# Performance work log

Hardware: AMD Instinct MI355X
Metric: run time of the kernel (lower is better)

## Reference

```python
import jax, jax.numpy as jnp
import numpy as np

N = 30000
SLOPE = 0.2  # PyG GATConv default negative_slope


def _gat_conv(x, src, dst, W, a_src, a_dst, b, heads, out_ch, concat):
    """PyG GATConv (add_self_loops already applied), eval mode (no dropout).
    x: [N, F_in]; src/dst: [E] int; W: [F_in, heads*out_ch];
    a_src/a_dst: [heads, out_ch]; b: [heads*out_ch] or [out_ch]."""
    n = x.shape[0]
    h = (x @ W).reshape(n, heads, out_ch)              # [N, H, C]
    al_src = jnp.sum(h * a_src, axis=-1)               # [N, H]
    al_dst = jnp.sum(h * a_dst, axis=-1)               # [N, H]
    e = jax.nn.leaky_relu(al_src[src] + al_dst[dst], SLOPE)  # [E, H]
    # segment softmax over incoming edges of each destination node
    m = jax.ops.segment_max(e, dst, num_segments=n)
    ex = jnp.exp(e - m[dst])
    denom = jax.ops.segment_sum(ex, dst, num_segments=n)
    alpha = ex / (denom[dst] + 1e-16)                  # [E, H]
    msg = h[src] * alpha[..., None]                    # [E, H, C]
    out = jax.ops.segment_sum(msg, dst, num_segments=n)  # [N, H, C]
    out = out.reshape(n, heads * out_ch) if concat else out.mean(axis=1)
    return out + b


def setup_inputs() -> dict:
    key = jax.random.key(0)
    ks = jax.random.split(key, 20)
    E = 480000
    IN, H0, H1, LAT = 256, 64, 128, 32
    HEADS = 4
    x = jax.random.normal(ks[0], (N, IN), dtype=jnp.float32)
    edge_index = jax.random.randint(ks[1], (2, E), 0, N, dtype=jnp.int32)

    def gp(k, fin, heads, outc, concat):
        k1, k2, k3, k4 = jax.random.split(k, 4)
        s = 0.1
        W = jax.random.normal(k1, (fin, heads * outc), dtype=jnp.float32) * s
        a_s = jax.random.normal(k2, (heads, outc), dtype=jnp.float32) * s
        a_d = jax.random.normal(k3, (heads, outc), dtype=jnp.float32) * s
        b = jax.random.normal(k4, (heads * outc if concat else outc,), dtype=jnp.float32) * s
        return W, a_s, a_d, b

    W1, as1, ad1, b1 = gp(ks[2], IN, HEADS, H0, True)
    W2, as2, ad2, b2 = gp(ks[3], H0 * HEADS, HEADS, H1, True)
    Wm, asm, adm, bm = gp(ks[4], H1 * HEADS, HEADS, LAT, False)
    Wl, asl, adl, bl = gp(ks[5], H1 * HEADS, HEADS, LAT, False)
    return dict(x=x, edge_index=edge_index,
                W1=W1, as1=as1, ad1=ad1, b1=b1,
                W2=W2, as2=as2, ad2=ad2, b2=b2,
                Wm=Wm, asm=asm, adm=adm, bm=bm,
                Wl=Wl, asl=asl, adl=adl, bl=bl)


def reference(x, edge_index, W1, as1, ad1, b1, W2, as2, ad2, b2,
              Wm, asm, adm, bm, Wl, asl, adl, bl):
    n = x.shape[0]
    # add self loops (PyG GATConv default)
    loop = jnp.arange(n, dtype=edge_index.dtype)
    src = jnp.concatenate([edge_index[0], loop])
    dst = jnp.concatenate([edge_index[1], loop])

    out = _gat_conv(x, src, dst, W1, as1, ad1, b1, heads=4, out_ch=64, concat=True)
    out = jax.nn.relu(out)
    out = _gat_conv(out, src, dst, W2, as2, ad2, b2, heads=4, out_ch=128, concat=True)
    out = jax.nn.relu(out)
    # F.dropout with training=False (eval) is identity
    z_mean = _gat_conv(out, src, dst, Wm, asm, adm, bm, heads=4, out_ch=32, concat=False)
    z_logstd = _gat_conv(out, src, dst, Wl, asl, adl, bl, heads=4, out_ch=32, concat=False)
    return z_mean, z_logstd
```

## Files before the change

### kernel.cpp

```cpp
#include <hip/hip_runtime.h>
#include <cstddef>

typedef __attribute__((ext_vector_type(8))) short short8;
typedef __attribute__((ext_vector_type(4))) float f32x4;
typedef __attribute__((ext_vector_type(8))) _Float16 half8;
typedef __attribute__((ext_vector_type(2))) _Float16 half2v;

union H8 { half8 v; half2v p[4]; unsigned int w[4]; };
union W1H2 { unsigned int w; half2v p; };

__device__ __forceinline__ unsigned short f2h(float f) {
    union { _Float16 h; unsigned short u; } x; x.h = (_Float16)f; return x.u;
}
__device__ __forceinline__ float h2f(unsigned short u) {
    union { unsigned short u; _Float16 h; } x; x.u = u; return (float)x.h;
}
__device__ __forceinline__ float lrelu(float v) { return v > 0.f ? v : 0.2f * v; }


__global__ void count_edges_kernel(const int* __restrict__ ei, int E, int N,
                                   int* __restrict__ cnt) {
    int e = blockIdx.x * blockDim.x + threadIdx.x;
    if (e >= E + N) return;
    int d = (e < E) ? ei[E + e] : (e - E);
    atomicAdd(&cnt[d], 1);
}


__global__ void scan_p1_kernel(const int* __restrict__ cnt, int* __restrict__ rp,
                               int* __restrict__ bsum, int n) {
    __shared__ int sh[256];
    int t = threadIdx.x, i = blockIdx.x * 256 + t;
    sh[t] = (i < n) ? cnt[i] : 0;
    __syncthreads();
    for (int off = 1; off < 256; off <<= 1) {
        int u = (t >= off) ? sh[t - off] : 0;
        __syncthreads();
        sh[t] += u;
        __syncthreads();
    }
    if (i < n) rp[i + 1] = sh[t];
    if (t == 255) bsum[blockIdx.x] = sh[255];
}

__global__ void scan_p2_kernel(int* __restrict__ bsum, int nb) {
    __shared__ int sh[256];
    int t = threadIdx.x;
    sh[t] = (t < nb) ? bsum[t] : 0;
    __syncthreads();
    for (int off = 1; off < 256; off <<= 1) {
        int u = (t >= off) ? sh[t - off] : 0;
        __syncthreads();
        sh[t] += u;
        __syncthreads();
    }
    if (t < nb) bsum[t] = (t == 0) ? 0 : sh[t - 1];
}

__global__ void scan_p3_kernel(int* __restrict__ rp, const int* __restrict__ bsum,
                               int* __restrict__ cnt, int n) {
    int i = blockIdx.x * 256 + threadIdx.x;
    if (i < n) {
        rp[i + 1] += bsum[blockIdx.x];
        cnt[i] = 0;
    }
    if (i == 0) rp[0] = 0;
}

__global__ void scatter_edges_kernel(const int* __restrict__ ei, int E, int N,
                                     const int* __restrict__ rp, int* __restrict__ cur,
                                     int* __restrict__ csrc) {
    int e = blockIdx.x * blockDim.x + threadIdx.x;
    if (e >= E + N) return;
    int s, d;
    if (e < E) { s = ei[e]; d = ei[E + e]; } else { s = e - E; d = s; }
    int pos = rp[d] + atomicAdd(&cur[d], 1);
    csrc[pos] = s;
}


__global__ void f32_to_f16_pad4_kernel(const float* __restrict__ in,
                                       unsigned short* __restrict__ out,
                                       int rows, int cols, int padRows) {
    int i = blockIdx.x * blockDim.x + threadIdx.x;
    int total = (padRows * cols) >> 2;
    if (i >= total) return;
    int r = (i * 4) / cols;
    ushort4 o;
    if (r < rows) {
        float4 v = *(const float4*)(in + (size_t)i * 4);
        o = make_ushort4(f2h(v.x), f2h(v.y), f2h(v.z), f2h(v.w));
    } else {
        o = make_ushort4(0, 0, 0, 0);
    }
    *(ushort4*)(out + (size_t)i * 4) = o;
}

__global__ void transpose_all_kernel(
    const float* __restrict__ W1, const float* __restrict__ W2,
    const float* __restrict__ Wm, const float* __restrict__ Wl,
    unsigned short* __restrict__ W1t, unsigned short* __restrict__ W2t,
    unsigned short* __restrict__ WmlT) {
    int i = blockIdx.x * blockDim.x + threadIdx.x;
    if (i < 65536) {
        int k = i >> 8, n = i & 255;
        W1t[(size_t)n * 256 + k] = f2h(W1[i]);
    } else if (i < 65536 + 131072) {
        int j = i - 65536;
        int k = j >> 9, n = j & 511;
        W2t[(size_t)n * 256 + k] = f2h(W2[j]);
    } else if (i < 65536 + 131072 + 65536) {
        int j = i - 196608;
        int k = j >> 7, n = j & 127;
        WmlT[(size_t)n * 512 + k] = f2h(Wm[j]);
    } else if (i < 65536 + 131072 + 131072) {
        int j = i - 262144;
        int k = j >> 7, n = j & 127;
        WmlT[(size_t)(128 + n) * 512 + k] = f2h(Wl[j]);
    }
}


__global__ __launch_bounds__(256) void gemm_f16_kernel(
    const unsigned short* __restrict__ A, const unsigned short* __restrict__ Bt,
    unsigned short* __restrict__ C, int M, int K, int Nc,
    float* __restrict__ al_s, float* __restrict__ al_d,
    const float* __restrict__ aslo, const float* __restrict__ adlo,
    const float* __restrict__ ashi, const float* __restrict__ adhi,
    int csplit, int Chead, int H) {
    __shared__ short As[64 * 32];
    __shared__ short Bs[128 * 32];
    __shared__ float salS[64][4];
    __shared__ float salD[64][4];
    int tid = threadIdx.x;
    int bm = blockIdx.y * 64;
    int bn = blockIdx.x * 128;
    int wave = tid >> 6, lane = tid & 63;
    int wm = (wave >> 1) * 32, wn = (wave & 1) * 64;
    int lm = lane & 15, lq = lane >> 4;

    f32x4 acc[2][4] = {};

    int c0 = tid, c1 = tid + 256;
    const unsigned short* Ap0 = A + (size_t)(bm + (c0 >> 2)) * K + (c0 & 3) * 8;
    const unsigned short* Bp0 = Bt + (size_t)(bn + (c0 >> 2)) * K + (c0 & 3) * 8;
    const unsigned short* Bp1 = Bt + (size_t)(bn + (c1 >> 2)) * K + (c1 & 3) * 8;

    short8 a0 = *(const short8*)(Ap0);
    short8 b0 = *(const short8*)(Bp0);
    short8 b1 = *(const short8*)(Bp1);

    for (int kk = 0; kk < K; kk += 32) {
        __syncthreads();
        *(short8*)&As[c0 * 8] = a0;
        *(short8*)&Bs[c0 * 8] = b0;
        *(short8*)&Bs[c1 * 8] = b1;
        if (kk + 32 < K) {
            a0 = *(const short8*)(Ap0 + kk + 32);
            b0 = *(const short8*)(Bp0 + kk + 32);
            b1 = *(const short8*)(Bp1 + kk + 32);
        }
        __syncthreads();
        half8 af[2], bf[4];
#pragma unroll
        for (int t = 0; t < 2; t++)
            af[t] = *(const half8*)&As[(wm + t * 16 + lm) * 32 + lq * 8];
#pragma unroll
        for (int t = 0; t < 4; t++)
            bf[t] = *(const half8*)&Bs[(wn + t * 16 + lm) * 32 + lq * 8];
#pragma unroll
        for (int tm = 0; tm < 2; tm++)
#pragma unroll
            for (int tn = 0; tn < 4; tn++)
                acc[tm][tn] = __builtin_amdgcn_mfma_f32_16x16x32_f16(
                    af[tm], bf[tn], acc[tm][tn], 0, 0, 0);
    }

#pragma unroll
    for (int tm = 0; tm < 2; tm++) {
#pragma unroll
        for (int r = 0; r < 4; r++) {
            int row = bm + wm + tm * 16 + lq * 4 + r;
            if (row < M) {
#pragma unroll
                for (int tn = 0; tn < 4; tn++) {
                    int col = bn + wn + tn * 16 + lm;
                    C[(size_t)row * Nc + col] = f2h(acc[tm][tn][r]);
                }
            }
        }
    }

    float asv[4], adv[4];
#pragma unroll
    for (int tn = 0; tn < 4; tn++) {
        int col = bn + wn + tn * 16 + lm;
        bool hi = col >= csplit;
        int cc = hi ? col - csplit : col;
        asv[tn] = hi ? ashi[cc] : aslo[cc];
        adv[tn] = hi ? adhi[cc] : adlo[cc];
    }
    int gb = wn >> 5;
#pragma unroll
    for (int tm = 0; tm < 2; tm++) {
#pragma unroll
        for (int r = 0; r < 4; r++) {
#pragma unroll
            for (int p = 0; p < 2; p++) {
                float s1 = acc[tm][2 * p][r] * asv[2 * p]
                         + acc[tm][2 * p + 1][r] * asv[2 * p + 1];
                float s2 = acc[tm][2 * p][r] * adv[2 * p]
                         + acc[tm][2 * p + 1][r] * adv[2 * p + 1];
#pragma unroll
                for (int off = 8; off >= 1; off >>= 1) {
                    s1 += __shfl_xor(s1, off);
                    s2 += __shfl_xor(s2, off);
                }
                if (lm == 0) {
                    int rl = wm + tm * 16 + lq * 4 + r;
                    salS[rl][gb + p] = s1;
                    salD[rl][gb + p] = s2;
                }
            }
        }
    }
    __syncthreads();
    if (tid < 64) {
        int row = bm + tid;
        if (row < M) {
            int hb = bn / Chead;
            int HB = 128 / Chead;
            int GH = Chead >> 5;
            for (int i = 0; i < HB; i++) {
                float ss = 0.f, sd = 0.f;
                for (int j = 0; j < GH; j++) {
                    ss += salS[tid][i * GH + j];
                    sd += salD[tid][i * GH + j];
                }
                al_s[(size_t)row * H + hb + i] = ss;
                al_d[(size_t)row * H + hb + i] = sd;
            }
        }
    }
}


template <int H4>
__global__ __launch_bounds__(256) void alpha_kernel(
    const int* __restrict__ rp, const int* __restrict__ csrc,
    const float* __restrict__ al_s, const float* __restrict__ al_d,
    unsigned short* __restrict__ alphaT, int Ep, int N) {
    const int H = 4 * H4;
    int wv = threadIdx.x >> 6;
    int lane = threadIdx.x & 63;
    int n = blockIdx.x * 4 + wv;
    if (n >= N) return;
    int beg = rp[n], end = rp[n + 1];
    int deg = end - beg;

    float ad[H];
#pragma unroll
    for (int g = 0; g < H4; g++)
        *(float4*)&ad[g * 4] = *(const float4*)(al_d + (size_t)n * H + g * 4);

    if (deg <= 64) {
        bool act = lane < deg;
        int s = act ? csrc[beg + lane] : 0;
        float v[H], m[H], ex[H], sum[H];
#pragma unroll
        for (int g = 0; g < H4; g++) {
            float4 as = *(const float4*)(al_s + (size_t)s * H + g * 4);
            v[g * 4 + 0] = lrelu(as.x + ad[g * 4 + 0]);
            v[g * 4 + 1] = lrelu(as.y + ad[g * 4 + 1]);
            v[g * 4 + 2] = lrelu(as.z + ad[g * 4 + 2]);
            v[g * 4 + 3] = lrelu(as.w + ad[g * 4 + 3]);
        }
#pragma unroll
        for (int j = 0; j < H; j++) m[j] = act ? v[j] : -3.402823466e38f;
#pragma unroll
        for (int off = 32; off >= 1; off >>= 1)
#pragma unroll
            for (int j = 0; j < H; j++) m[j] = fmaxf(m[j], __shfl_xor(m[j], off));
#pragma unroll
        for (int j = 0; j < H; j++) {
            ex[j] = act ? __expf(v[j] - m[j]) : 0.f;
            sum[j] = ex[j];
        }
#pragma unroll
        for (int off = 32; off >= 1; off >>= 1)
#pragma unroll
            for (int j = 0; j < H; j++) sum[j] += __shfl_xor(sum[j], off);
        if (act) {
#pragma unroll
            for (int j = 0; j < H; j++)
                alphaT[(size_t)j * Ep + beg + lane] = f2h(ex[j] / (sum[j] + 1e-16f));
        }
    } else {
        float m[H], sum[H];
#pragma unroll
        for (int j = 0; j < H; j++) m[j] = -3.402823466e38f;
        for (int e = beg + lane; e < end; e += 64) {
            int s = csrc[e];
#pragma unroll
            for (int g = 0; g < H4; g++) {
                float4 as = *(const float4*)(al_s + (size_t)s * H + g * 4);
                m[g * 4 + 0] = fmaxf(m[g * 4 + 0], lrelu(as.x + ad[g * 4 + 0]));
                m[g * 4 + 1] = fmaxf(m[g * 4 + 1], lrelu(as.y + ad[g * 4 + 1]));
                m[g * 4 + 2] = fmaxf(m[g * 4 + 2], lrelu(as.z + ad[g * 4 + 2]));
                m[g * 4 + 3] = fmaxf(m[g * 4 + 3], lrelu(as.w + ad[g * 4 + 3]));
            }
        }
#pragma unroll
        for (int off = 32; off >= 1; off >>= 1)
#pragma unroll
            for (int j = 0; j < H; j++) m[j] = fmaxf(m[j], __shfl_xor(m[j], off));
#pragma unroll
        for (int j = 0; j < H; j++) sum[j] = 0.f;
        for (int e = beg + lane; e < end; e += 64) {
            int s = csrc[e];
#pragma unroll
            for (int g = 0; g < H4; g++) {
                float4 as = *(const float4*)(al_s + (size_t)s * H + g * 4);
                sum[g * 4 + 0] += __expf(lrelu(as.x + ad[g * 4 + 0]) - m[g * 4 + 0]);
                sum[g * 4 + 1] += __expf(lrelu(as.y + ad[g * 4 + 1]) - m[g * 4 + 1]);
                sum[g * 4 + 2] += __expf(lrelu(as.z + ad[g * 4 + 2]) - m[g * 4 + 2]);
                sum[g * 4 + 3] += __expf(lrelu(as.w + ad[g * 4 + 3]) - m[g * 4 + 3]);
            }
        }
#pragma unroll
        for (int off = 32; off >= 1; off >>= 1)
#pragma unroll
            for (int j = 0; j < H; j++) sum[j] += __shfl_xor(sum[j], off);
        float r[H];
#pragma unroll
        for (int j = 0; j < H; j++) r[j] = 1.0f / (sum[j] + 1e-16f);
        for (int e = beg + lane; e < end; e += 64) {
            int s = csrc[e];
#pragma unroll
            for (int g = 0; g < H4; g++) {
                float4 as = *(const float4*)(al_s + (size_t)s * H + g * 4);
                alphaT[(size_t)(g * 4 + 0) * Ep + e] =
                    f2h(__expf(lrelu(as.x + ad[g * 4 + 0]) - m[g * 4 + 0]) * r[g * 4 + 0]);
                alphaT[(size_t)(g * 4 + 1) * Ep + e] =
                    f2h(__expf(lrelu(as.y + ad[g * 4 + 1]) - m[g * 4 + 1]) * r[g * 4 + 1]);
                alphaT[(size_t)(g * 4 + 2) * Ep + e] =
                    f2h(__expf(lrelu(as.z + ad[g * 4 + 2]) - m[g * 4 + 2]) * r[g * 4 + 2]);
                alphaT[(size_t)(g * 4 + 3) * Ep + e] =
                    f2h(__expf(lrelu(as.w + ad[g * 4 + 3]) - m[g * 4 + 3]) * r[g * 4 + 3]);
            }
        }
    }
}


template <int NS, int HC, int C>
__global__ __launch_bounds__(256) void agg_stage_kernel(
    const int* __restrict__ rp, const int* __restrict__ csrc,
    const unsigned short* __restrict__ alphaT, int Ep,
    const unsigned short* __restrict__ h, const float* __restrict__ bias,
    unsigned short* __restrict__ out, int N) {
    constexpr int NG = 32;
    constexpr int MAXE = 1024;
    __shared__ int lds_rp[NG + 1];
    __shared__ uint2 lds_ea[MAXE];
    int tid = threadIdx.x;
    int bs = blockIdx.x % NS;
    int g0 = (blockIdx.x / NS) * NG;
    const int hd = (bs * 64) / C;
    if (tid <= NG) {
        int nn = g0 + tid;
        lds_rp[tid] = rp[nn <= N ? nn : N];
    }
    __syncthreads();
    int e0 = lds_rp[0], span = lds_rp[NG] - e0;
    const unsigned short* at = alphaT + (size_t)hd * Ep + e0;
    bool fits = span <= MAXE;
    if (fits) {
        for (int i = tid; i < span; i += 256) {
            unsigned int off = (unsigned int)csrc[e0 + i] * (unsigned int)(HC * 2);
            unsigned int a = at[i];
            lds_ea[i] = make_uint2(off, a | (a << 16));
        }
    }
    __syncthreads();

    int grp = tid >> 3;
    int lg = tid & 7;
    int n = g0 + grp;
    if (n >= N) return;
    int ch = bs * 64 + lg * 8;
    const unsigned int lo = (unsigned int)ch * 2;
    const char* hb = (const char*)h;
    H8 A; A.v = half8{};

    if (fits) {
        int t = lds_rp[grp] - e0, end = lds_rp[grp + 1] - e0;
        for (; t + 3 < end; t += 4) {
            uint2 ea0 = lds_ea[t],     ea1 = lds_ea[t + 1];
            uint2 ea2 = lds_ea[t + 2], ea3 = lds_ea[t + 3];
            H8 h0, h1, h2, h3;
            h0.v = *(const half8*)(hb + (ea0.x + lo));
            h1.v = *(const half8*)(hb + (ea1.x + lo));
            h2.v = *(const half8*)(hb + (ea2.x + lo));
            h3.v = *(const half8*)(hb + (ea3.x + lo));
            W1H2 a0, a1, a2, a3;
            a0.w = ea0.y; a1.w = ea1.y; a2.w = ea2.y; a3.w = ea3.y;
#pragma unroll
            for (int i = 0; i < 4; i++) A.p[i] += h0.p[i] * a0.p;
#pragma unroll
            for (int i = 0; i < 4; i++) A.p[i] += h1.p[i] * a1.p;
#pragma unroll
            for (int i = 0; i < 4; i++) A.p[i] += h2.p[i] * a2.p;
#pragma unroll
            for (int i = 0; i < 4; i++) A.p[i] += h3.p[i] * a3.p;
        }
        for (; t < end; t++) {
            uint2 ea0 = lds_ea[t];
            W1H2 a0; a0.w = ea0.y;
            H8 h0; h0.v = *(const half8*)(hb + (ea0.x + lo));
#pragma unroll
            for (int i = 0; i < 4; i++) A.p[i] += h0.p[i] * a0.p;
        }
    } else {
        const unsigned short* atg = alphaT + (size_t)hd * Ep;
        for (int t = lds_rp[grp]; t < lds_rp[grp + 1]; t++) {
            unsigned int off = (unsigned int)csrc[t] * (unsigned int)(HC * 2);
            unsigned int a = atg[t];
            W1H2 a0; a0.w = a | (a << 16);
            H8 h0; h0.v = *(const half8*)(hb + (off + lo));
#pragma unroll
            for (int i = 0; i < 4; i++) A.p[i] += h0.p[i] * a0.p;
        }
    }

    short8 o;
#pragma unroll
    for (int i = 0; i < 8; i++)
        o[i] = (short)f2h(fmaxf((float)A.v[i] + bias[ch + i], 0.f));
    *(short8*)(out + (size_t)n * HC + ch) = o;
}


__global__ __launch_bounds__(256) void agg_mean_stage_kernel(
    const int* __restrict__ rp, const int* __restrict__ csrc,
    const unsigned short* __restrict__ alphaT, int Ep,
    const unsigned short* __restrict__ h,
    const float* __restrict__ bias1, const float* __restrict__ bias2,
    float* __restrict__ out1, float* __restrict__ out2, int N) {
    constexpr int NG = 16;
    constexpr int MAXE = 1024;
    __shared__ int lds_rp[NG + 1];
    __shared__ unsigned int lds_off[MAXE];
    __shared__ unsigned int lds_aw[4][MAXE];
    int tid = threadIdx.x;
    int o = blockIdx.x & 1;
    int g0 = (blockIdx.x >> 1) * NG;
    if (tid <= NG) {
        int nn = g0 + tid;
        lds_rp[tid] = rp[nn <= N ? nn : N];
    }
    __syncthreads();
    int e0 = lds_rp[0], span = lds_rp[NG] - e0;
    bool fits = span <= MAXE;
    if (fits) {
        for (int i = tid; i < span; i += 256)
            lds_off[i] = (unsigned int)csrc[e0 + i] * 512u;
#pragma unroll
        for (int hh = 0; hh < 4; hh++) {
            const unsigned short* at = alphaT + (size_t)(o * 4 + hh) * Ep + e0;
            for (int i = tid; i < span; i += 256) {
                unsigned int a = at[i];
                lds_aw[hh][i] = a | (a << 16);
            }
        }
    }
    __syncthreads();

    int grp = tid >> 4;
    int cg = tid & 15;
    int hh = cg >> 2;
    int n = g0 + grp;
    if (n >= N) return;
    int ch = o * 128 + cg * 8;
    const unsigned int lo = (unsigned int)ch * 2;
    const char* hb = (const char*)h;
    H8 A; A.v = half8{};

    if (fits) {
        int t = lds_rp[grp] - e0, end = lds_rp[grp + 1] - e0;
        for (; t + 3 < end; t += 4) {
            unsigned int o0 = lds_off[t],     o1 = lds_off[t + 1];
            unsigned int o2 = lds_off[t + 2], o3 = lds_off[t + 3];
            H8 h0, h1, h2, h3;
            h0.v = *(const half8*)(hb + (o0 + lo));
            h1.v = *(const half8*)(hb + (o1 + lo));
            h2.v = *(const half8*)(hb + (o2 + lo));
            h3.v = *(const half8*)(hb + (o3 + lo));
            W1H2 a0, a1, a2, a3;
            a0.w = lds_aw[hh][t];     a1.w = lds_aw[hh][t + 1];
            a2.w = lds_aw[hh][t + 2]; a3.w = lds_aw[hh][t + 3];
#pragma unroll
            for (int i = 0; i < 4; i++) A.p[i] += h0.p[i] * a0.p;
#pragma unroll
            for (int i = 0; i < 4; i++) A.p[i] += h1.p[i] * a1.p;
#pragma unroll
            for (int i = 0; i < 4; i++) A.p[i] += h2.p[i] * a2.p;
#pragma unroll
            for (int i = 0; i < 4; i++) A.p[i] += h3.p[i] * a3.p;
        }
        for (; t < end; t++) {
            W1H2 a0; a0.w = lds_aw[hh][t];
            H8 h0; h0.v = *(const half8*)(hb + (lds_off[t] + lo));
#pragma unroll
            for (int i = 0; i < 4; i++) A.p[i] += h0.p[i] * a0.p;
        }
    } else {
        const unsigned short* atg = alphaT + (size_t)(o * 4 + hh) * Ep;
        for (int t = lds_rp[grp]; t < lds_rp[grp + 1]; t++) {
            unsigned int off = (unsigned int)csrc[t] * 512u;
            unsigned int a = atg[t];
            W1H2 a0; a0.w = a | (a << 16);
            H8 h0; h0.v = *(const half8*)(hb + (off + lo));
#pragma unroll
            for (int i = 0; i < 4; i++) A.p[i] += h0.p[i] * a0.p;
        }
    }

    float f[8];
#pragma unroll
    for (int i = 0; i < 8; i++) f[i] = (float)A.v[i];
#pragma unroll
    for (int off = 4; off <= 8; off <<= 1)
#pragma unroll
        for (int i = 0; i < 8; i++) f[i] += __shfl_xor(f[i], off);
    if (cg < 4) {
        const float* bb = o ? bias2 : bias1;
        float* op = o ? out2 : out1;
        int wc = cg * 8;
        float4 r0, r1;
        r0.x = f[0] * 0.25f + bb[wc + 0];
        r0.y = f[1] * 0.25f + bb[wc + 1];
        r0.z = f[2] * 0.25f + bb[wc + 2];
        r0.w = f[3] * 0.25f + bb[wc + 3];
        r1.x = f[4] * 0.25f + bb[wc + 4];
        r1.y = f[5] * 0.25f + bb[wc + 5];
        r1.z = f[6] * 0.25f + bb[wc + 6];
        r1.w = f[7] * 0.25f + bb[wc + 7];
        *(float4*)(op + (size_t)n * 32 + wc) = r0;
        *(float4*)(op + (size_t)n * 32 + wc + 4) = r1;
    }
}


extern "C" void kernel_launch(void* const* d_in, const int* in_sizes, int n_in,
                              void* d_out, int out_size, void* d_ws, size_t ws_size,
                              hipStream_t stream) {
    (void)n_in; (void)out_size; (void)ws_size;
    const float* x   = (const float*)d_in[0];
    const int*   ei  = (const int*)d_in[1];
    const float* W1  = (const float*)d_in[2];
    const float* as1 = (const float*)d_in[3];
    const float* ad1 = (const float*)d_in[4];
    const float* b1  = (const float*)d_in[5];
    const float* W2  = (const float*)d_in[6];
    const float* as2 = (const float*)d_in[7];
    const float* ad2 = (const float*)d_in[8];
    const float* b2  = (const float*)d_in[9];
    const float* Wm  = (const float*)d_in[10];
    const float* a_sm = (const float*)d_in[11];
    const float* a_dm = (const float*)d_in[12];
    const float* bm  = (const float*)d_in[13];
    const float* Wl  = (const float*)d_in[14];
    const float* a_sl = (const float*)d_in[15];
    const float* a_dl = (const float*)d_in[16];
    const float* bl  = (const float*)d_in[17];
    float* outp = (float*)d_out;

    const int N  = in_sizes[0] / 256;
    const int E  = in_sizes[1] / 2;
    const int ET = E + N;
    const int gM128 = (N + 127) / 128;
    const int Mp = gM128 * 128;
    const int gM64 = (N + 63) / 64;
    const int nSB = (N + 255) / 256;

    auto align_up = [](size_t v) { return (v + 255) & ~(size_t)255; };
    char* w = (char*)d_ws;
    int* row_ptr = (int*)w;  w += align_up((size_t)(N + 1) * 4);
    int* cnt     = (int*)w;  w += align_up((size_t)N * 4);
    int* bsum    = (int*)w;  w += align_up((size_t)nSB * 4);
    int* csrc    = (int*)w;  w += align_up((size_t)ET * 4);
    float* al_s  = (float*)w; w += align_up((size_t)N * 8 * 4);
    float* al_d  = (float*)w; w += align_up((size_t)N * 8 * 4);
    unsigned short* xb   = (unsigned short*)w; w += align_up((size_t)Mp * 256 * 2);
    unsigned short* W1t  = (unsigned short*)w; w += align_up((size_t)256 * 256 * 2);
    unsigned short* W2t  = (unsigned short*)w; w += align_up((size_t)512 * 256 * 2);
    unsigned short* WmlT = (unsigned short*)w; w += align_up((size_t)256 * 512 * 2);
    unsigned short* bufH = (unsigned short*)w; w += align_up((size_t)Mp * 512 * 2);
    unsigned short* bufO = (unsigned short*)w; w += align_up((size_t)Mp * 512 * 2);
    unsigned short* alphaT = xb;

    int gzE = (ET + 255) / 256;
    hipMemsetAsync(cnt, 0, (size_t)N * 4, stream);
    count_edges_kernel<<<gzE, 256, 0, stream>>>(ei, E, N, cnt);
    scan_p1_kernel<<<nSB, 256, 0, stream>>>(cnt, row_ptr, bsum, N);
    scan_p2_kernel<<<1, 256, 0, stream>>>(bsum, nSB);
    scan_p3_kernel<<<nSB, 256, 0, stream>>>(row_ptr, bsum, cnt, N);
    scatter_edges_kernel<<<gzE, 256, 0, stream>>>(ei, E, N, row_ptr, cnt, csrc);

    f32_to_f16_pad4_kernel<<<((Mp * 256 / 4) + 255) / 256, 256, 0, stream>>>(
        x, xb, N, 256, Mp);
    transpose_all_kernel<<<(393216 + 255) / 256, 256, 0, stream>>>(
        W1, W2, Wm, Wl, W1t, W2t, WmlT);

    int gF = (N + 3) / 4;
    int gB = (N + 31) / 32;
    int gB2 = (N + 15) / 16;

    gemm_f16_kernel<<<dim3(2, gM64), 256, 0, stream>>>(
        xb, W1t, bufH, N, 256, 256, al_s, al_d, as1, ad1, as1, ad1, 256, 64, 4);
    alpha_kernel<1><<<gF, 256, 0, stream>>>(row_ptr, csrc, al_s, al_d, alphaT, ET, N);
    agg_stage_kernel<4, 256, 64><<<4 * gB, 256, 0, stream>>>(
        row_ptr, csrc, alphaT, ET, bufH, b1, bufO, N);

    gemm_f16_kernel<<<dim3(4, gM64), 256, 0, stream>>>(
        bufO, W2t, bufH, N, 256, 512, al_s, al_d, as2, ad2, as2, ad2, 512, 128, 4);
    alpha_kernel<1><<<gF, 256, 0, stream>>>(row_ptr, csrc, al_s, al_d, alphaT, ET, N);
    agg_stage_kernel<8, 512, 128><<<8 * gB, 256, 0, stream>>>(
        row_ptr, csrc, alphaT, ET, bufH, b2, bufO, N);

    gemm_f16_kernel<<<dim3(2, gM64), 256, 0, stream>>>(
        bufO, WmlT, bufH, N, 512, 256, al_s, al_d, a_sm, a_dm, a_sl, a_dl, 128, 32, 8);
    alpha_kernel<2><<<gF, 256, 0, stream>>>(row_ptr, csrc, al_s, al_d, alphaT, ET, N);
    agg_mean_stage_kernel<<<2 * gB2, 256, 0, stream>>>(
        row_ptr, csrc, alphaT, ET, bufH, bm, bl, outp, outp + (size_t)N * 32, N);
}
```

Measured before the change: 405.0 us.

## Merge scan and prep kernels, load GEMM tiles directly into LDS

Folds the block-sum scan into the final scan pass, where each block rescans the block sums itself. It also merges the x conversion and weight transpose into one launch, cutting two kernel launches overall. Separately, the GEMM's register-staged prefetch is replaced with direct global-to-LDS loads, which removes VGPR staging but also drops the software prefetch overlap across iterations.

New measurement: 403.3 us. About the same (-0.4%).

```diff
diff --git a/kernel.cpp b/kernel.cpp
--- a/kernel.cpp
+++ b/kernel.cpp
@@ -16,6 +16,12 @@
     union { unsigned short u; _Float16 h; } x; x.u = u; return (float)x.h;
 }
 __device__ __forceinline__ float lrelu(float v) { return v > 0.f ? v : 0.2f * v; }
+
+__device__ __forceinline__ void gl_lds16(const void* g, void* l) {
+    __builtin_amdgcn_global_load_lds(
+        (const __attribute__((address_space(1))) void*)g,
+        (__attribute__((address_space(3))) void*)l, 16, 0, 0);
+}
 
 
 __global__ void count_edges_kernel(const int* __restrict__ ei, int E, int N,
@@ -43,7 +49,8 @@
     if (t == 255) bsum[blockIdx.x] = sh[255];
 }
 
-__global__ void scan_p2_kernel(int* __restrict__ bsum, int nb) {
+__global__ void scan_p3_kernel(int* __restrict__ rp, const int* __restrict__ bsum,
+                               int* __restrict__ cnt, int n, int nb) {
     __shared__ int sh[256];
     int t = threadIdx.x;
     sh[t] = (t < nb) ? bsum[t] : 0;
@@ -54,14 +61,10 @@
         sh[t] += u;
         __syncthreads();
     }
-    if (t < nb) bsum[t] = (t == 0) ? 0 : sh[t - 1];
-}
-
-__global__ void scan_p3_kernel(int* __restrict__ rp, const int* __restrict__ bsum,
-                               int* __restrict__ cnt, int n) {
-    int i = blockIdx.x * 256 + threadIdx.x;
+    int off = (blockIdx.x == 0) ? 0 : sh[blockIdx.x - 1];
+    int i = blockIdx.x * 256 + t;
     if (i < n) {
-        rp[i + 1] += bsum[blockIdx.x];
+        rp[i + 1] += off;
         cnt[i] = 0;
     }
     if (i == 0) rp[0] = 0;
@@ -79,29 +82,29 @@
 }
 
 
-__global__ void f32_to_f16_pad4_kernel(const float* __restrict__ in,
-                                       unsigned short* __restrict__ out,
-                                       int rows, int cols, int padRows) {
-    int i = blockIdx.x * blockDim.x + threadIdx.x;
-    int total = (padRows * cols) >> 2;
-    if (i >= total) return;
-    int r = (i * 4) / cols;
-    ushort4 o;
-    if (r < rows) {
-        float4 v = *(const float4*)(in + (size_t)i * 4);
-        o = make_ushort4(f2h(v.x), f2h(v.y), f2h(v.z), f2h(v.w));
-    } else {
-        o = make_ushort4(0, 0, 0, 0);
-    }
-    *(ushort4*)(out + (size_t)i * 4) = o;
-}
-
-__global__ void transpose_all_kernel(
+__global__ void prep_kernel(
+    const float* __restrict__ x, unsigned short* __restrict__ xb,
+    int rows, int cols, int padRows,
     const float* __restrict__ W1, const float* __restrict__ W2,
     const float* __restrict__ Wm, const float* __restrict__ Wl,
     unsigned short* __restrict__ W1t, unsigned short* __restrict__ W2t,
-    unsigned short* __restrict__ WmlT) {
-    int i = blockIdx.x * blockDim.x + threadIdx.x;
+    unsigned short* __restrict__ WmlT, int xBlocks) {
+    if ((int)blockIdx.x < xBlocks) {
+        int i = blockIdx.x * blockDim.x + threadIdx.x;
+        int total = (padRows * cols) >> 2;
+        if (i >= total) return;
+        int r = (i * 4) / cols;
+        ushort4 o;
+        if (r < rows) {
+            float4 v = *(const float4*)(x + (size_t)i * 4);
+            o = make_ushort4(f2h(v.x), f2h(v.y), f2h(v.z), f2h(v.w));
+        } else {
+            o = make_ushort4(0, 0, 0, 0);
+        }
+        *(ushort4*)(xb + (size_t)i * 4) = o;
+        return;
+    }
+    int i = (blockIdx.x - xBlocks) * blockDim.x + threadIdx.x;
     if (i < 65536) {
         int k = i >> 8, n = i & 255;
         W1t[(size_t)n * 256 + k] = f2h(W1[i]);
@@ -146,20 +149,11 @@
     const unsigned short* Bp0 = Bt + (size_t)(bn + (c0 >> 2)) * K + (c0 & 3) * 8;
     const unsigned short* Bp1 = Bt + (size_t)(bn + (c1 >> 2)) * K + (c1 & 3) * 8;
 
-    short8 a0 = *(const short8*)(Ap0);
-    short8 b0 = *(const short8*)(Bp0);
-    short8 b1 = *(const short8*)(Bp1);
-
     for (int kk = 0; kk < K; kk += 32) {
         __syncthreads();
-        *(short8*)&As[c0 * 8] = a0;
-        *(short8*)&Bs[c0 * 8] = b0;
-        *(short8*)&Bs[c1 * 8] = b1;
-        if (kk + 32 < K) {
-            a0 = *(const short8*)(Ap0 + kk + 32);
-            b0 = *(const short8*)(Bp0 + kk + 32);
-            b1 = *(const short8*)(Bp1 + kk + 32);
-        }
+        gl_lds16(Ap0 + kk, &As[c0 * 8]);
+        gl_lds16(Bp0 + kk, &Bs[c0 * 8]);
+        gl_lds16(Bp1 + kk, &Bs[c1 * 8]);
         __syncthreads();
         half8 af[2], bf[4];
 #pragma unroll
@@ -604,14 +598,13 @@
     hipMemsetAsync(cnt, 0, (size_t)N * 4, stream);
     count_edges_kernel<<<gzE, 256, 0, stream>>>(ei, E, N, cnt);
     scan_p1_kernel<<<nSB, 256, 0, stream>>>(cnt, row_ptr, bsum, N);
-    scan_p2_kernel<<<1, 256, 0, stream>>>(bsum, nSB);
-    scan_p3_kernel<<<nSB, 256, 0, stream>>>(row_ptr, bsum, cnt, N);
+    scan_p3_kernel<<<nSB, 256, 0, stream>>>(row_ptr, bsum, cnt, N, nSB);
     scatter_edges_kernel<<<gzE, 256, 0, stream>>>(ei, E, N, row_ptr, cnt, csrc);
 
-    f32_to_f16_pad4_kernel<<<((Mp * 256 / 4) + 255) / 256, 256, 0, stream>>>(
-        x, xb, N, 256, Mp);
-    transpose_all_kernel<<<(393216 + 255) / 256, 256, 0, stream>>>(
-        W1, W2, Wm, Wl, W1t, W2t, WmlT);
+    int xBlocks = ((Mp * 256 / 4) + 255) / 256;
+    int wBlocks = (393216 + 255) / 256;
+    prep_kernel<<<xBlocks + wBlocks, 256, 0, stream>>>(
+        x, xb, N, 256, Mp, W1, W2, Wm, Wl, W1t, W2t, WmlT, xBlocks);
 
     int gF = (N + 3) / 4;
     int gB = (N + 31) / 32;
```
